# Kernel optimization log

Hardware: AMD Instinct MI355X
Metric: run time of the kernel (lower is better)

## Reference

```python
import jax, jax.numpy as jnp
import numpy as np
from jax import lax

SAMPLE_RATE = 44100.0

def _shelf_coeffs(gain_db, fc, q, sr, high):
    # RBJ cookbook shelf biquad; high=True -> high_shelf, else low_shelf
    A = 10.0 ** (gain_db / 40.0)
    w0 = 2.0 * jnp.pi * (fc / sr)
    alpha = jnp.sin(w0) / (2.0 * q)
    c = jnp.cos(w0)
    sA = jnp.sqrt(A)
    sgn = 1.0 if high else -1.0
    b0 = A * (A + 1 + sgn * (A - 1) * c + 2 * sA * alpha)
    b1 = -2.0 * sgn * A * (A - 1 + sgn * (A + 1) * c)
    b2 = A * (A + 1 + sgn * (A - 1) * c - 2 * sA * alpha)
    a0 = A + 1 - sgn * (A - 1) * c + 2 * sA * alpha
    a1 = 2.0 * sgn * (A - 1 - sgn * (A + 1) * c)
    a2 = A + 1 - sgn * (A - 1) * c - 2 * sA * alpha
    b = jnp.stack([b0, b1, b2]) / a0
    a = jnp.stack([a0, a1, a2]) / a0
    return b, a

def _peaking_coeffs(gain_db, fc, q, sr):
    A = 10.0 ** (gain_db / 40.0)
    w0 = 2.0 * jnp.pi * (fc / sr)
    alpha = jnp.sin(w0) / (2.0 * q)
    c = jnp.cos(w0)
    b0 = 1 + alpha * A
    b1 = -2.0 * c
    b2 = 1 - alpha * A
    a0 = 1 + alpha / A
    a1 = -2.0 * c
    a2 = 1 - alpha / A
    b = jnp.stack([b0, b1, b2]) / a0
    a = jnp.stack([a0, a1, a2]) / a0
    return b, a

def _biquad_lfilter(b, a, x):
    # scipy.signal.lfilter with zero initial conditions, transposed DF-II.
    # x: (chs, T); state s: (chs, 2)
    b0, b1, b2 = b[0], b[1], b[2]
    a1, a2 = a[1], a[2]
    def step(s, xn):  # xn: (chs,)
        s1, s2 = s[:, 0], s[:, 1]
        yn = b0 * xn + s1
        s1n = b1 * xn - a1 * yn + s2
        s2n = b2 * xn - a2 * yn
        return jnp.stack([s1n, s2n], axis=1), yn
    s0 = jnp.zeros((x.shape[0], 2), x.dtype)
    _, y = lax.scan(step, s0, x.T)  # y: (T, chs)
    return y.T

def setup_inputs() -> dict:
    key = jax.random.key(0)
    x = jax.random.normal(key, (8, 2097152), dtype=jnp.float32)
    # rows: [low_shelf, band1, band2, band3, high_shelf]; cols: [gain_db, cutoff_hz, Q]
    eq_params = jnp.array([
        [3.0, 100.0, 0.9],
        [-2.5, 400.0, 1.2],
        [4.0, 1000.0, 2.0],
        [-5.0, 4000.0, 0.7],
        [2.5, 12000.0, 0.707],
    ], dtype=jnp.float32)
    return {"x": x, "eq_params": eq_params}

def reference(x, eq_params):
    sr = SAMPLE_RATE
    # low shelf
    b, a = _shelf_coeffs(eq_params[0, 0], eq_params[0, 1], eq_params[0, 2], sr, high=False)
    y = _biquad_lfilter(b, a, x)
    # 3 peaking bands
    for i in range(1, 4):
        b, a = _peaking_coeffs(eq_params[i, 0], eq_params[i, 1], eq_params[i, 2], sr)
        y = _biquad_lfilter(b, a, y)
    # high shelf
    b, a = _shelf_coeffs(eq_params[4, 0], eq_params[4, 1], eq_params[4, 2], sr, high=True)
    y = _biquad_lfilter(b, a, y)
    return y.astype(jnp.float32)
```

## Files before the change

### kernel.cpp

```cpp
#include <hip/hip_runtime.h>

#define SRATE 44100.0
#define WIN 16
#define NWIN 4
#define STRIDE 17
#define NBLK 1024
#define BLK_PER_CH 128

#ifndef M_PI
#define M_PI 3.14159265358979323846
#endif

struct CoefD { double b0, b1, b2, a1, a2; };

__device__ void cascade_step_d(const CoefD* cf, double* s, double x) {
    double u = x;
    #pragma unroll
    for (int i = 0; i < 5; i++) {
        double y   = cf[i].b0 * u + s[2*i];
        double s1n = cf[i].b1 * u - cf[i].a1 * y + s[2*i+1];
        double s2n = cf[i].b2 * u - cf[i].a2 * y;
        s[2*i]   = s1n;
        s[2*i+1] = s2n;
        u = y;
    }
}

__global__ __launch_bounds__(128) void k0_setup(const float* __restrict__ eqp,
                                                float* __restrict__ coef_f,
                                                float* __restrict__ mats_f) {
    __shared__ CoefD cf[5];
    __shared__ double M[100];
    int t = threadIdx.x;

    if (t < 5) {
        int i = t;
        double g  = (double)eqp[i*3 + 0];
        double fc = (double)eqp[i*3 + 1];
        double q  = (double)eqp[i*3 + 2];
        double A  = pow(10.0, g / 40.0);
        double w0 = 2.0 * M_PI * (fc / SRATE);
        double al = sin(w0) / (2.0 * q);
        double c  = cos(w0);
        double b0, b1, b2, a0, a1, a2;
        if (i == 0 || i == 4) {
            double sgn = (i == 4) ? 1.0 : -1.0;
            double sA = sqrt(A);
            b0 = A * ((A + 1.0) + sgn * (A - 1.0) * c + 2.0 * sA * al);
            b1 = -2.0 * sgn * A * ((A - 1.0) + sgn * (A + 1.0) * c);
            b2 = A * ((A + 1.0) + sgn * (A - 1.0) * c - 2.0 * sA * al);
            a0 = (A + 1.0) - sgn * (A - 1.0) * c + 2.0 * sA * al;
            a1 = 2.0 * sgn * ((A - 1.0) - sgn * (A + 1.0) * c);
            a2 = (A + 1.0) - sgn * (A - 1.0) * c - 2.0 * sA * al;
        } else {
            b0 = 1.0 + al * A; b1 = -2.0 * c; b2 = 1.0 - al * A;
            a0 = 1.0 + al / A; a1 = -2.0 * c; a2 = 1.0 - al / A;
        }
        cf[i].b0 = b0 / a0; cf[i].b1 = b1 / a0; cf[i].b2 = b2 / a0;
        cf[i].a1 = a1 / a0; cf[i].a2 = a2 / a0;
        coef_f[i*5 + 0] = (float)(b0 / a0);
        coef_f[i*5 + 1] = (float)(b1 / a0);
        coef_f[i*5 + 2] = (float)(b2 / a0);
        coef_f[i*5 + 3] = (float)(a1 / a0);
        coef_f[i*5 + 4] = (float)(a2 / a0);
    }
    __syncthreads();

    if (t < 10) {
        double s[10];
        for (int k = 0; k < 10; k++) s[k] = (k == t) ? 1.0 : 0.0;
        cascade_step_d(cf, s, 0.0);
        for (int r = 0; r < 10; r++) M[r*10 + t] = s[r];
    }
    __syncthreads();

    for (int k = 1; k <= 20; k++) {
        double val = 0.0;
        if (t < 100) {
            int r = t / 10, c = t % 10;
            for (int j = 0; j < 10; j++) val += M[r*10 + j] * M[j*10 + c];
        }
        __syncthreads();
        if (t < 100) {
            M[t] = val;
            if (k >= 6 && k <= 13) mats_f[(k-6)*100 + t]         = (float)val;
            if (k >= 14)           mats_f[800 + (k-14)*100 + t]  = (float)val;
        }
        __syncthreads();
    }
}

__global__ __launch_bounds__(256, 4) void k1_fused(const float* __restrict__ x,
                                                   const float* __restrict__ coef,
                                                   const float* __restrict__ mats_f,
                                                   float* __restrict__ ibuf,
                                                   float* __restrict__ abuf) {
    __shared__ union SmemU {
        float stage[2][256 * STRIDE];
        float buf[256][11];
    } sm;
    int t = threadIdx.x, b = blockIdx.x;

    float cb0[5], cb1[5], cb2[5], ca1[5], ca2[5];
    #pragma unroll
    for (int i = 0; i < 5; i++) {
        cb0[i] = coef[i*5+0]; cb1[i] = coef[i*5+1]; cb2[i] = coef[i*5+2];
        ca1[i] = coef[i*5+3]; ca2[i] = coef[i*5+4];
    }
    const float4* x4 = (const float4*)x;
    const size_t base4 = (size_t)b * 4096;
    const int cb = t >> 2, q = t & 3;

    float4 rr[4];
    #pragma unroll
    for (int k = 0; k < 4; k++)
        rr[k] = x4[base4 + (size_t)(cb + 64*k) * 16 + q];
    #pragma unroll
    for (int k = 0; k < 4; k++) {
        int o = (cb + 64*k) * STRIDE + q*4;
        sm.stage[0][o+0] = rr[k].x; sm.stage[0][o+1] = rr[k].y;
        sm.stage[0][o+2] = rr[k].z; sm.stage[0][o+3] = rr[k].w;
    }
    __syncthreads();

    float s[10];
    #pragma unroll
    for (int k = 0; k < 10; k++) s[k] = 0.0f;

    for (int w = 0; w < NWIN; w++) {
        if (w + 1 < NWIN) {
            #pragma unroll
            for (int k = 0; k < 4; k++)
                rr[k] = x4[base4 + (size_t)(cb + 64*k) * 16 + (w+1)*4 + q];
        }
        const float* cur = sm.stage[w & 1] + t * STRIDE;
        #pragma unroll
        for (int i = 0; i < WIN; i++) {
            float u = cur[i];
            #pragma unroll
            for (int st = 0; st < 5; st++) {
                float y  = fmaf(cb0[st], u, s[2*st]);
                float t1 = fmaf(cb1[st], u, s[2*st+1]);
                s[2*st+1] = fmaf(-ca2[st], y, cb2[st] * u);
                s[2*st]   = fmaf(-ca1[st], y, t1);
                u = y;
            }
        }
        if (w + 1 < NWIN) {
            float* nb = sm.stage[(w+1) & 1];
            #pragma unroll
            for (int k = 0; k < 4; k++) {
                int o = (cb + 64*k) * STRIDE + q*4;
                nb[o+0] = rr[k].x; nb[o+1] = rr[k].y;
                nb[o+2] = rr[k].z; nb[o+3] = rr[k].w;
            }
        }
        __syncthreads();
    }

    #pragma unroll
    for (int r = 0; r < 10; r++) sm.buf[t][r] = s[r];
    __syncthreads();

    for (int d = 0; d < 8; d++) {
        const float* __restrict__ Mg = mats_f + d*100;
        float nv[10];
        bool act = (t >= (1 << d));
        if (act) {
            int src = t - (1 << d);
            float bs[10];
            #pragma unroll
            for (int k = 0; k < 10; k++) bs[k] = sm.buf[src][k];
            #pragma unroll
            for (int r = 0; r < 10; r++) {
                float acc = s[r];
                #pragma unroll
                for (int k = 0; k < 10; k++)
                    acc = fmaf(Mg[r*10 + k], bs[k], acc);
                nv[r] = acc;
            }
        }
        __syncthreads();
        if (act) {
            #pragma unroll
            for (int r = 0; r < 10; r++) { s[r] = nv[r]; sm.buf[t][r] = nv[r]; }
        }
        __syncthreads();
    }

    #pragma unroll
    for (int r = 0; r < 10; r++)
        ibuf[(size_t)b * 2560 + r * 256 + t] = (t > 0) ? sm.buf[t-1][r] : 0.0f;
    if (t == 255) {
        #pragma unroll
        for (int r = 0; r < 10; r++) abuf[b * 10 + r] = s[r];
    }
}

__global__ __launch_bounds__(256, 4) void k3_final(const float* __restrict__ x,
                                                   const float* __restrict__ coef,
                                                   const float* __restrict__ mats_f,
                                                   const float* __restrict__ ibuf,
                                                   const float* __restrict__ abuf,
                                                   float* __restrict__ out) {
    __shared__ union SmemU {
        float inb[2][256 * STRIDE];
        struct { float pad[256 * STRIDE]; float sbuf[128][11]; } scn;
    } sm;
    int t = threadIdx.x, b = blockIdx.x;
    const int ch = b >> 7;
    const int ci = b & 127;

    const float4* x4 = (const float4*)x;
    float4* o4 = (float4*)out;
    const size_t base4 = (size_t)b * 4096;
    const int cb = t >> 2, q = t & 3;

    float4 rr[4];
    #pragma unroll
    for (int k = 0; k < 4; k++)
        rr[k] = x4[base4 + (size_t)(cb + 64*k) * 16 + q];

    float cb0[5], cb1[5], cb2[5], ca1[5], ca2[5];
    #pragma unroll
    for (int i = 0; i < 5; i++) {
        cb0[i] = coef[i*5+0]; cb1[i] = coef[i*5+1]; cb2[i] = coef[i*5+2];
        ca1[i] = coef[i*5+3]; ca2[i] = coef[i*5+4];
    }

    float s[10];
    #pragma unroll
    for (int r = 0; r < 10; r++)
        s[r] = ibuf[(size_t)b * 2560 + r * 256 + t];

    #pragma unroll
    for (int k = 0; k < 4; k++) {
        int o = (cb + 64*k) * STRIDE + q*4;
        sm.inb[0][o+0] = rr[k].x; sm.inb[0][o+1] = rr[k].y;
        sm.inb[0][o+2] = rr[k].z; sm.inb[0][o+3] = rr[k].w;
    }
    for (int idx = t; idx < 1280; idx += 256)
        sm.scn.sbuf[idx / 10][idx % 10] = abuf[(size_t)ch * 1280 + idx];
    __syncthreads();

    float v[10];
    if (t < 128) {
        #pragma unroll
        for (int r = 0; r < 10; r++) v[r] = sm.scn.sbuf[t][r];
    }
    for (int e = 0; e < 7; e++) {
        const float* __restrict__ Qg = mats_f + 800 + e*100;
        float nv[10];
        bool act = (t < 128) && (t >= (1 << e));
        if (act) {
            int src = t - (1 << e);
            float bs[10];
            #pragma unroll
            for (int k = 0; k < 10; k++) bs[k] = sm.scn.sbuf[src][k];
            #pragma unroll
            for (int r = 0; r < 10; r++) {
                float acc = v[r];
                #pragma unroll
                for (int k = 0; k < 10; k++)
                    acc = fmaf(Qg[r*10 + k], bs[k], acc);
                nv[r] = acc;
            }
        }
        __syncthreads();
        if (act) {
            #pragma unroll
            for (int r = 0; r < 10; r++) { v[r] = nv[r]; sm.scn.sbuf[t][r] = nv[r]; }
        }
        __syncthreads();
    }

    float bp[10];
    #pragma unroll
    for (int r = 0; r < 10; r++)
        bp[r] = (ci > 0) ? sm.scn.sbuf[ci-1][r] : 0.0f;
    __syncthreads();

    for (int d = 0; d < 8; d++) {
        const float* __restrict__ Mg = mats_f + d*100;
        float wv[10];
        #pragma unroll
        for (int r = 0; r < 10; r++) {
            float acc = 0.0f;
            #pragma unroll
            for (int k = 0; k < 10; k++)
                acc = fmaf(Mg[r*10 + k], bp[k], acc);
            wv[r] = acc;
        }
        bool bit = (t >> d) & 1;
        #pragma unroll
        for (int r = 0; r < 10; r++) bp[r] = bit ? wv[r] : bp[r];
    }
    #pragma unroll
    for (int r = 0; r < 10; r++) s[r] += bp[r];

    for (int w = 0; w < NWIN; w++) {
        if (w + 1 < NWIN) {
            #pragma unroll
            for (int k = 0; k < 4; k++)
                rr[k] = x4[base4 + (size_t)(cb + 64*k) * 16 + (w+1)*4 + q];
        }
        float* cur = sm.inb[w & 1] + t * STRIDE;
        #pragma unroll
        for (int i = 0; i < WIN; i++) {
            float u = cur[i];
            #pragma unroll
            for (int st = 0; st < 5; st++) {
                float y  = fmaf(cb0[st], u, s[2*st]);
                float t1 = fmaf(cb1[st], u, s[2*st+1]);
                s[2*st+1] = fmaf(-ca2[st], y, cb2[st] * u);
                s[2*st]   = fmaf(-ca1[st], y, t1);
                u = y;
            }
            cur[i] = u;
        }
        if (w + 1 < NWIN) {
            float* nb = sm.inb[(w+1) & 1];
            #pragma unroll
            for (int k = 0; k < 4; k++) {
                int o = (cb + 64*k) * STRIDE + q*4;
                nb[o+0] = rr[k].x; nb[o+1] = rr[k].y;
                nb[o+2] = rr[k].z; nb[o+3] = rr[k].w;
            }
        }
        __syncthreads();

        const float* sb = sm.inb[w & 1];
        #pragma unroll
        for (int k = 0; k < 4; k++) {
            int o = (cb + 64*k) * STRIDE + q*4;
            float4 ov = make_float4(sb[o+0], sb[o+1], sb[o+2], sb[o+3]);
            o4[base4 + (size_t)(cb + 64*k) * 16 + (size_t)w*4 + q] = ov;
        }
    }
}

extern "C" void kernel_launch(void* const* d_in, const int* in_sizes, int n_in,
                              void* d_out, int out_size, void* d_ws, size_t ws_size,
                              hipStream_t stream) {
    const float* x   = (const float*)d_in[0];
    const float* eqp = (const float*)d_in[1];
    float* out = (float*)d_out;
    char* ws = (char*)d_ws;

    float* coef_f = (float*)ws;
    float* mats_f = (float*)(ws + 256);
    float* ibuf   = (float*)(ws + 8192);
    float* abuf   = (float*)(ws + 8192 + 10485760);

    hipLaunchKernelGGL(k0_setup, dim3(1), dim3(128), 0, stream, eqp, coef_f, mats_f);
    hipLaunchKernelGGL(k1_fused, dim3(NBLK), dim3(256), 0, stream, x, coef_f, mats_f, ibuf, abuf);
    hipLaunchKernelGGL(k3_final, dim3(NBLK), dim3(256), 0, stream,
                       x, coef_f, mats_f, ibuf, abuf, out);
}
```

Measured before the change: 173.7 us.

## Restructure scan: per-block table rebuild, direct register loads, separate carry-scan kernel

Removes the single-block setup kernel. Every block now recomputes the filter coefficients and matrix-power tables into shared memory, overlapping that with its input loads. Each thread now handles 32 contiguous samples loaded straight into registers as float4, replacing the shared-memory staging and double buffering. Blocks per channel double to 256, and a small 8-block kernel does the cross-block carry scan instead of repeating it inside every final block. The trade-off is redundant double-precision table building in every block (20 serial matrix squarings with barriers) and uncoalesced strided float4 access.

Result: slower. 242.2 us (+39.4%).

```diff
diff --git a/kernel.cpp b/kernel.cpp
--- a/kernel.cpp
+++ b/kernel.cpp
@@ -1,38 +1,20 @@
 #include <hip/hip_runtime.h>
 
 #define SRATE 44100.0
-#define WIN 16
-#define NWIN 4
-#define STRIDE 17
-#define NBLK 1024
-#define BLK_PER_CH 128
-
 #ifndef M_PI
 #define M_PI 3.14159265358979323846
 #endif
 
-struct CoefD { double b0, b1, b2, a1, a2; };
-
-__device__ void cascade_step_d(const CoefD* cf, double* s, double x) {
-    double u = x;
-    #pragma unroll
-    for (int i = 0; i < 5; i++) {
-        double y   = cf[i].b0 * u + s[2*i];
-        double s1n = cf[i].b1 * u - cf[i].a1 * y + s[2*i+1];
-        double s2n = cf[i].b2 * u - cf[i].a2 * y;
-        s[2*i]   = s1n;
-        s[2*i+1] = s2n;
-        u = y;
-    }
-}
-
-__global__ __launch_bounds__(128) void k0_setup(const float* __restrict__ eqp,
-                                                float* __restrict__ coef_f,
-                                                float* __restrict__ mats_f) {
-    __shared__ CoefD cf[5];
-    __shared__ double M[100];
+#define CHUNK 32
+#define THREADS 256
+#define NBLK 2048
+#define BLK_PER_CH 256
+#define MSTRIDE 12
+
+__device__ __forceinline__ void build_block_tables(const float* __restrict__ eqp,
+                                                   double* cfd, double* Md,
+                                                   float* cfs, float* Mf, int klo) {
     int t = threadIdx.x;
-
     if (t < 5) {
         int i = t;
         double g  = (double)eqp[i*3 + 0];
@@ -56,21 +38,27 @@
             b0 = 1.0 + al * A; b1 = -2.0 * c; b2 = 1.0 - al * A;
             a0 = 1.0 + al / A; a1 = -2.0 * c; a2 = 1.0 - al / A;
         }
-        cf[i].b0 = b0 / a0; cf[i].b1 = b1 / a0; cf[i].b2 = b2 / a0;
-        cf[i].a1 = a1 / a0; cf[i].a2 = a2 / a0;
-        coef_f[i*5 + 0] = (float)(b0 / a0);
-        coef_f[i*5 + 1] = (float)(b1 / a0);
-        coef_f[i*5 + 2] = (float)(b2 / a0);
-        coef_f[i*5 + 3] = (float)(a1 / a0);
-        coef_f[i*5 + 4] = (float)(a2 / a0);
+        cfd[i*5+0] = b0/a0; cfd[i*5+1] = b1/a0; cfd[i*5+2] = b2/a0;
+        cfd[i*5+3] = a1/a0; cfd[i*5+4] = a2/a0;
+        cfs[i*5+0] = (float)(b0/a0); cfs[i*5+1] = (float)(b1/a0);
+        cfs[i*5+2] = (float)(b2/a0); cfs[i*5+3] = (float)(a1/a0);
+        cfs[i*5+4] = (float)(a2/a0);
     }
     __syncthreads();
 
     if (t < 10) {
         double s[10];
+        #pragma unroll
         for (int k = 0; k < 10; k++) s[k] = (k == t) ? 1.0 : 0.0;
-        cascade_step_d(cf, s, 0.0);
-        for (int r = 0; r < 10; r++) M[r*10 + t] = s[r];
+        double u = 0.0;
+        #pragma unroll
+        for (int i = 0; i < 5; i++) {
+            double y   = cfd[i*5+0] * u + s[2*i];
+            double s1n = cfd[i*5+1] * u - cfd[i*5+3] * y + s[2*i+1];
+            double s2n = cfd[i*5+2] * u - cfd[i*5+4] * y;
+            s[2*i] = s1n; s[2*i+1] = s2n; u = y;
+        }
+        for (int r = 0; r < 10; r++) Md[r*10 + t] = s[r];
     }
     __syncthreads();
 
@@ -78,65 +66,56 @@
         double val = 0.0;
         if (t < 100) {
             int r = t / 10, c = t % 10;
-            for (int j = 0; j < 10; j++) val += M[r*10 + j] * M[j*10 + c];
+            #pragma unroll
+            for (int j = 0; j < 10; j++) val += Md[r*10 + j] * Md[j*10 + c];
         }
         __syncthreads();
         if (t < 100) {
-            M[t] = val;
-            if (k >= 6 && k <= 13) mats_f[(k-6)*100 + t]         = (float)val;
-            if (k >= 14)           mats_f[800 + (k-14)*100 + t]  = (float)val;
-        }
-        __syncthreads();
-    }
-}
-
-__global__ __launch_bounds__(256, 4) void k1_fused(const float* __restrict__ x,
-                                                   const float* __restrict__ coef,
-                                                   const float* __restrict__ mats_f,
-                                                   float* __restrict__ ibuf,
-                                                   float* __restrict__ abuf) {
-    __shared__ union SmemU {
-        float stage[2][256 * STRIDE];
-        float buf[256][11];
-    } sm;
+            Md[t] = val;
+            int d = k - klo;
+            if (d >= 0 && d < 8)
+                Mf[d*120 + (t/10)*MSTRIDE + (t%10)] = (float)val;
+        }
+        __syncthreads();
+    }
+}
+
+__global__ __launch_bounds__(256, 6) void kA(const float* __restrict__ x,
+                                             const float* __restrict__ eqp,
+                                             float* __restrict__ ibuf,
+                                             float* __restrict__ abuf) {
+    __shared__ double cfd[25];
+    __shared__ double Md[100];
+    __shared__ float  cfs[25];
+    __shared__ __align__(16) float Mf[960];
+    __shared__ float  buf[256][11];
+
     int t = threadIdx.x, b = blockIdx.x;
 
+    const float4* x4 = (const float4*)x + ((size_t)b * 256 + t) * 8;
+    float4 rr[8];
+    #pragma unroll
+    for (int j = 0; j < 8; j++) rr[j] = x4[j];
+
+    build_block_tables(eqp, cfd, Md, cfs, Mf, 5);
+
     float cb0[5], cb1[5], cb2[5], ca1[5], ca2[5];
     #pragma unroll
     for (int i = 0; i < 5; i++) {
-        cb0[i] = coef[i*5+0]; cb1[i] = coef[i*5+1]; cb2[i] = coef[i*5+2];
-        ca1[i] = coef[i*5+3]; ca2[i] = coef[i*5+4];
-    }
-    const float4* x4 = (const float4*)x;
-    const size_t base4 = (size_t)b * 4096;
-    const int cb = t >> 2, q = t & 3;
-
-    float4 rr[4];
-    #pragma unroll
-    for (int k = 0; k < 4; k++)
-        rr[k] = x4[base4 + (size_t)(cb + 64*k) * 16 + q];
-    #pragma unroll
-    for (int k = 0; k < 4; k++) {
-        int o = (cb + 64*k) * STRIDE + q*4;
-        sm.stage[0][o+0] = rr[k].x; sm.stage[0][o+1] = rr[k].y;
-        sm.stage[0][o+2] = rr[k].z; sm.stage[0][o+3] = rr[k].w;
-    }
-    __syncthreads();
+        cb0[i] = cfs[i*5+0]; cb1[i] = cfs[i*5+1]; cb2[i] = cfs[i*5+2];
+        ca1[i] = cfs[i*5+3]; ca2[i] = cfs[i*5+4];
+    }
 
     float s[10];
     #pragma unroll
     for (int k = 0; k < 10; k++) s[k] = 0.0f;
 
-    for (int w = 0; w < NWIN; w++) {
-        if (w + 1 < NWIN) {
-            #pragma unroll
-            for (int k = 0; k < 4; k++)
-                rr[k] = x4[base4 + (size_t)(cb + 64*k) * 16 + (w+1)*4 + q];
-        }
-        const float* cur = sm.stage[w & 1] + t * STRIDE;
-        #pragma unroll
-        for (int i = 0; i < WIN; i++) {
-            float u = cur[i];
+    #pragma unroll
+    for (int j = 0; j < 8; j++) {
+        float xs[4] = { rr[j].x, rr[j].y, rr[j].z, rr[j].w };
+        #pragma unroll
+        for (int i = 0; i < 4; i++) {
+            float u = xs[i];
             #pragma unroll
             for (int st = 0; st < 5; st++) {
                 float y  = fmaf(cb0[st], u, s[2*st]);
@@ -146,168 +125,157 @@
                 u = y;
             }
         }
-        if (w + 1 < NWIN) {
-            float* nb = sm.stage[(w+1) & 1];
-            #pragma unroll
-            for (int k = 0; k < 4; k++) {
-                int o = (cb + 64*k) * STRIDE + q*4;
-                nb[o+0] = rr[k].x; nb[o+1] = rr[k].y;
-                nb[o+2] = rr[k].z; nb[o+3] = rr[k].w;
-            }
-        }
-        __syncthreads();
-    }
-
-    #pragma unroll
-    for (int r = 0; r < 10; r++) sm.buf[t][r] = s[r];
+    }
+
+    #pragma unroll
+    for (int r = 0; r < 10; r++) buf[t][r] = s[r];
     __syncthreads();
 
+    #pragma unroll 1
     for (int d = 0; d < 8; d++) {
-        const float* __restrict__ Mg = mats_f + d*100;
+        int lvl = d * 120;
+        int src = t - (1 << d);
+        int sc  = src < 0 ? 0 : src;
+        float bs[10];
+        #pragma unroll
+        for (int r = 0; r < 10; r++) bs[r] = buf[sc][r];
         float nv[10];
-        bool act = (t >= (1 << d));
-        if (act) {
-            int src = t - (1 << d);
-            float bs[10];
-            #pragma unroll
-            for (int k = 0; k < 10; k++) bs[k] = sm.buf[src][k];
-            #pragma unroll
-            for (int r = 0; r < 10; r++) {
-                float acc = s[r];
-                #pragma unroll
-                for (int k = 0; k < 10; k++)
-                    acc = fmaf(Mg[r*10 + k], bs[k], acc);
-                nv[r] = acc;
-            }
-        }
-        __syncthreads();
-        if (act) {
-            #pragma unroll
-            for (int r = 0; r < 10; r++) { s[r] = nv[r]; sm.buf[t][r] = nv[r]; }
-        }
+        #pragma unroll
+        for (int r = 0; r < 10; r++) {
+            float acc = s[r];
+            #pragma unroll
+            for (int k = 0; k < 10; k++)
+                acc = fmaf(Mf[lvl + r*MSTRIDE + k], bs[k], acc);
+            nv[r] = acc;
+        }
+        __syncthreads();
+        bool act = src >= 0;
+        #pragma unroll
+        for (int r = 0; r < 10; r++) { s[r] = act ? nv[r] : s[r]; buf[t][r] = s[r]; }
         __syncthreads();
     }
 
     #pragma unroll
     for (int r = 0; r < 10; r++)
-        ibuf[(size_t)b * 2560 + r * 256 + t] = (t > 0) ? sm.buf[t-1][r] : 0.0f;
+        ibuf[(size_t)b * 2560 + r * 256 + t] = (t > 0) ? buf[t-1][r] : 0.0f;
     if (t == 255) {
         #pragma unroll
         for (int r = 0; r < 10; r++) abuf[b * 10 + r] = s[r];
     }
 }
 
-__global__ __launch_bounds__(256, 4) void k3_final(const float* __restrict__ x,
-                                                   const float* __restrict__ coef,
-                                                   const float* __restrict__ mats_f,
-                                                   const float* __restrict__ ibuf,
-                                                   const float* __restrict__ abuf,
-                                                   float* __restrict__ out) {
-    __shared__ union SmemU {
-        float inb[2][256 * STRIDE];
-        struct { float pad[256 * STRIDE]; float sbuf[128][11]; } scn;
-    } sm;
+__global__ __launch_bounds__(256) void kB(const float* __restrict__ eqp,
+                                          const float* __restrict__ abuf,
+                                          float* __restrict__ bbuf) {
+    __shared__ double cfd[25];
+    __shared__ double Md[100];
+    __shared__ float  cfs[25];
+    __shared__ __align__(16) float Mf[960];
+    __shared__ float  buf[256][11];
+
+    int t = threadIdx.x, ch = blockIdx.x;
+    int g = ch * 256 + t;
+
+    float v[10];
+    #pragma unroll
+    for (int r = 0; r < 10; r++) v[r] = abuf[g * 10 + r];
+
+    build_block_tables(eqp, cfd, Md, cfs, Mf, 13);
+
+    #pragma unroll
+    for (int r = 0; r < 10; r++) buf[t][r] = v[r];
+    __syncthreads();
+
+    #pragma unroll 1
+    for (int e = 0; e < 8; e++) {
+        int lvl = e * 120;
+        int src = t - (1 << e);
+        int sc  = src < 0 ? 0 : src;
+        float bs[10];
+        #pragma unroll
+        for (int r = 0; r < 10; r++) bs[r] = buf[sc][r];
+        float nv[10];
+        #pragma unroll
+        for (int r = 0; r < 10; r++) {
+            float acc = v[r];
+            #pragma unroll
+            for (int k = 0; k < 10; k++)
+                acc = fmaf(Mf[lvl + r*MSTRIDE + k], bs[k], acc);
+            nv[r] = acc;
+        }
+        __syncthreads();
+        bool act = src >= 0;
+        #pragma unroll
+        for (int r = 0; r < 10; r++) { v[r] = act ? nv[r] : v[r]; buf[t][r] = v[r]; }
+        __syncthreads();
+    }
+
+    #pragma unroll
+    for (int r = 0; r < 10; r++)
+        bbuf[g * 10 + r] = (t > 0) ? buf[t-1][r] : 0.0f;
+}
+
+__global__ __launch_bounds__(256, 6) void kC(const float* __restrict__ x,
+                                             const float* __restrict__ eqp,
+                                             const float* __restrict__ ibuf,
+                                             const float* __restrict__ bbuf,
+                                             float* __restrict__ out) {
+    __shared__ double cfd[25];
+    __shared__ double Md[100];
+    __shared__ float  cfs[25];
+    __shared__ __align__(16) float Mf[960];
+
     int t = threadIdx.x, b = blockIdx.x;
-    const int ch = b >> 7;
-    const int ci = b & 127;
-
-    const float4* x4 = (const float4*)x;
-    float4* o4 = (float4*)out;
-    const size_t base4 = (size_t)b * 4096;
-    const int cb = t >> 2, q = t & 3;
-
-    float4 rr[4];
-    #pragma unroll
-    for (int k = 0; k < 4; k++)
-        rr[k] = x4[base4 + (size_t)(cb + 64*k) * 16 + q];
+
+    const float4* x4 = (const float4*)x + ((size_t)b * 256 + t) * 8;
+    float4 rr[8];
+    #pragma unroll
+    for (int j = 0; j < 8; j++) rr[j] = x4[j];
+
+    float sp[10];
+    #pragma unroll
+    for (int r = 0; r < 10; r++)
+        sp[r] = ibuf[(size_t)b * 2560 + r * 256 + t];
+    float bp[10];
+    #pragma unroll
+    for (int r = 0; r < 10; r++) bp[r] = bbuf[b * 10 + r];
+
+    build_block_tables(eqp, cfd, Md, cfs, Mf, 5);
 
     float cb0[5], cb1[5], cb2[5], ca1[5], ca2[5];
     #pragma unroll
     for (int i = 0; i < 5; i++) {
-        cb0[i] = coef[i*5+0]; cb1[i] = coef[i*5+1]; cb2[i] = coef[i*5+2];
-        ca1[i] = coef[i*5+3]; ca2[i] = coef[i*5+4];
-    }
-
-    float s[10];
-    #pragma unroll
-    for (int r = 0; r < 10; r++)
-        s[r] = ibuf[(size_t)b * 2560 + r * 256 + t];
-
-    #pragma unroll
-    for (int k = 0; k < 4; k++) {
-        int o = (cb + 64*k) * STRIDE + q*4;
-        sm.inb[0][o+0] = rr[k].x; sm.inb[0][o+1] = rr[k].y;
-        sm.inb[0][o+2] = rr[k].z; sm.inb[0][o+3] = rr[k].w;
-    }
-    for (int idx = t; idx < 1280; idx += 256)
-        sm.scn.sbuf[idx / 10][idx % 10] = abuf[(size_t)ch * 1280 + idx];
-    __syncthreads();
-
-    float v[10];
-    if (t < 128) {
-        #pragma unroll
-        for (int r = 0; r < 10; r++) v[r] = sm.scn.sbuf[t][r];
-    }
-    for (int e = 0; e < 7; e++) {
-        const float* __restrict__ Qg = mats_f + 800 + e*100;
-        float nv[10];
-        bool act = (t < 128) && (t >= (1 << e));
-        if (act) {
-            int src = t - (1 << e);
-            float bs[10];
-            #pragma unroll
-            for (int k = 0; k < 10; k++) bs[k] = sm.scn.sbuf[src][k];
-            #pragma unroll
-            for (int r = 0; r < 10; r++) {
-                float acc = v[r];
-                #pragma unroll
-                for (int k = 0; k < 10; k++)
-                    acc = fmaf(Qg[r*10 + k], bs[k], acc);
-                nv[r] = acc;
-            }
-        }
-        __syncthreads();
-        if (act) {
-            #pragma unroll
-            for (int r = 0; r < 10; r++) { v[r] = nv[r]; sm.scn.sbuf[t][r] = nv[r]; }
-        }
-        __syncthreads();
-    }
-
-    float bp[10];
-    #pragma unroll
-    for (int r = 0; r < 10; r++)
-        bp[r] = (ci > 0) ? sm.scn.sbuf[ci-1][r] : 0.0f;
-    __syncthreads();
-
+        cb0[i] = cfs[i*5+0]; cb1[i] = cfs[i*5+1]; cb2[i] = cfs[i*5+2];
+        ca1[i] = cfs[i*5+3]; ca2[i] = cfs[i*5+4];
+    }
+
+    #pragma unroll 1
     for (int d = 0; d < 8; d++) {
-        const float* __restrict__ Mg = mats_f + d*100;
+        int lvl = d * 120;
         float wv[10];
         #pragma unroll
         for (int r = 0; r < 10; r++) {
             float acc = 0.0f;
             #pragma unroll
             for (int k = 0; k < 10; k++)
-                acc = fmaf(Mg[r*10 + k], bp[k], acc);
+                acc = fmaf(Mf[lvl + r*MSTRIDE + k], bp[k], acc);
             wv[r] = acc;
         }
         bool bit = (t >> d) & 1;
         #pragma unroll
         for (int r = 0; r < 10; r++) bp[r] = bit ? wv[r] : bp[r];
     }
-    #pragma unroll
-    for (int r = 0; r < 10; r++) s[r] += bp[r];
-
-    for (int w = 0; w < NWIN; w++) {
-        if (w + 1 < NWIN) {
-            #pragma unroll
-            for (int k = 0; k < 4; k++)
-                rr[k] = x4[base4 + (size_t)(cb + 64*k) * 16 + (w+1)*4 + q];
-        }
-        float* cur = sm.inb[w & 1] + t * STRIDE;
-        #pragma unroll
-        for (int i = 0; i < WIN; i++) {
-            float u = cur[i];
+
+    float s[10];
+    #pragma unroll
+    for (int r = 0; r < 10; r++) s[r] = sp[r] + bp[r];
+
+    #pragma unroll
+    for (int j = 0; j < 8; j++) {
+        float xs[4] = { rr[j].x, rr[j].y, rr[j].z, rr[j].w };
+        #pragma unroll
+        for (int i = 0; i < 4; i++) {
+            float u = xs[i];
             #pragma unroll
             for (int st = 0; st < 5; st++) {
                 float y  = fmaf(cb0[st], u, s[2*st]);
@@ -316,27 +284,14 @@
                 s[2*st]   = fmaf(-ca1[st], y, t1);
                 u = y;
             }
-            cur[i] = u;
-        }
-        if (w + 1 < NWIN) {
-            float* nb = sm.inb[(w+1) & 1];
-            #pragma unroll
-            for (int k = 0; k < 4; k++) {
-                int o = (cb + 64*k) * STRIDE + q*4;
-                nb[o+0] = rr[k].x; nb[o+1] = rr[k].y;
-                nb[o+2] = rr[k].z; nb[o+3] = rr[k].w;
-            }
-        }
-        __syncthreads();
-
-        const float* sb = sm.inb[w & 1];
-        #pragma unroll
-        for (int k = 0; k < 4; k++) {
-            int o = (cb + 64*k) * STRIDE + q*4;
-            float4 ov = make_float4(sb[o+0], sb[o+1], sb[o+2], sb[o+3]);
-            o4[base4 + (size_t)(cb + 64*k) * 16 + (size_t)w*4 + q] = ov;
-        }
-    }
+            xs[i] = u;
+        }
+        rr[j] = make_float4(xs[0], xs[1], xs[2], xs[3]);
+    }
+
+    float4* o4 = (float4*)out + ((size_t)b * 256 + t) * 8;
+    #pragma unroll
+    for (int j = 0; j < 8; j++) o4[j] = rr[j];
 }
 
 extern "C" void kernel_launch(void* const* d_in, const int* in_sizes, int n_in,
@@ -347,13 +302,11 @@
     float* out = (float*)d_out;
     char* ws = (char*)d_ws;
 
-    float* coef_f = (float*)ws;
-    float* mats_f = (float*)(ws + 256);
-    float* ibuf   = (float*)(ws + 8192);
-    float* abuf   = (float*)(ws + 8192 + 10485760);
-
-    hipLaunchKernelGGL(k0_setup, dim3(1), dim3(128), 0, stream, eqp, coef_f, mats_f);
-    hipLaunchKernelGGL(k1_fused, dim3(NBLK), dim3(256), 0, stream, x, coef_f, mats_f, ibuf, abuf);
-    hipLaunchKernelGGL(k3_final, dim3(NBLK), dim3(256), 0, stream,
-                       x, coef_f, mats_f, ibuf, abuf, out);
-}
+    float* ibuf = (float*)ws;
+    float* abuf = (float*)(ws + 20971520);
+    float* bbuf = (float*)(ws + 20971520 + 81920);
+
+    hipLaunchKernelGGL(kA, dim3(NBLK), dim3(THREADS), 0, stream, x, eqp, ibuf, abuf);
+    hipLaunchKernelGGL(kB, dim3(8),    dim3(THREADS), 0, stream, eqp, abuf, bbuf);
+    hipLaunchKernelGGL(kC, dim3(NBLK), dim3(THREADS), 0, stream, x, eqp, ibuf, bbuf, out);
+}
```
